# Optimization experiments

Hardware: AMD Instinct MI355X
Metric: run time of the kernel (lower is better)

The kernel has to match this reference:

```python
import jax, jax.numpy as jnp
import numpy as np
from jax import lax

B, IN_N, MID_N, OUT_N, K, L, WH = 16, 256, 256, 256, 3, 4096, 1024
EPS = 1e-5


def att_conv(x, W, b=None):
    # x: [B, Cin, L], W: [B, Cout, Cin, K] -> per-sample conv1d, padding='same'
    pl, pr = (K - 1) // 2, K // 2
    xp = jnp.pad(x, ((0, 0), (0, 0), (pl, pr)))
    out = 0.
    for t in range(K):  # small fixed K, unrolled shifted-slice einsum
        out = out + jnp.einsum('bcl,boc->bol', lax.dynamic_slice_in_dim(xp, t, L, 2), W[..., t])
    if b is not None:
        out = out + b[:, :, None]
    return out


def batch_norm(x, w, b):
    # training-mode BN over (N, L) per channel, biased variance
    mean = x.mean((0, 2), keepdims=True)
    var = ((x - mean) ** 2).mean((0, 2), keepdims=True)
    return (x - mean) * (w[None, :, None] / jnp.sqrt(var + EPS)) + b[None, :, None]


def se_module(x, w1, b1, w2, b2):
    s = x.mean(2, keepdims=True)  # [B, C, 1]
    s = jax.nn.relu(jnp.einsum('bcl,oc->bol', s, w1) + b1[None, :, None])
    s = jax.nn.sigmoid(jnp.einsum('bcl,oc->bol', s, w2) + b2[None, :, None])
    return x * s


def setup_inputs() -> dict:
    key = jax.random.key(0)
    ks = jax.random.split(key, 16)
    f = lambda k, sh, sc=0.02: jax.random.normal(k, sh, jnp.float32) * sc
    return {
        'x': f(ks[0], (B, IN_N, L), 1.0),
        'att1': f(ks[1], (B, MID_N, WH), 1.0),
        'att2': f(ks[2], (B, MID_N, WH), 1.0),
        'att3': f(ks[3], (B, OUT_N, WH), 1.0),
        'w1_w': f(ks[4], (IN_N * K, WH)), 'w1_b': jnp.zeros((IN_N * K,), jnp.float32),
        'w2_w': f(ks[5], (MID_N * K, WH)), 'w2_b': jnp.zeros((MID_N * K,), jnp.float32),
        'w3_w': f(ks[6], (MID_N * K, WH)), 'w3_b': jnp.zeros((MID_N * K,), jnp.float32),
        'b1_w': f(ks[7], (1, WH)), 'b1_b': jnp.zeros((1,), jnp.float32),
        'bn2_w': jnp.full((MID_N,), 0.1, jnp.float32), 'bn2_b': jnp.zeros((MID_N,), jnp.float32),
        'bn3_w': jnp.full((OUT_N,), 0.1, jnp.float32), 'bn3_b': jnp.zeros((OUT_N,), jnp.float32),
        'se1_w': f(ks[8], (OUT_N, OUT_N)), 'se1_b': jnp.zeros((OUT_N,), jnp.float32),
        'se2_w': f(ks[9], (OUT_N, OUT_N)), 'se2_b': jnp.zeros((OUT_N,), jnp.float32),
    }


def reference(x, att1, att2, att3, w1_w, w1_b, w2_w, w2_b, w3_w, w3_b,
              b1_w, b1_b, bn2_w, bn2_b, bn3_w, bn3_b, se1_w, se1_b, se2_w, se2_b):
    shortcut = x  # in_n == out_n, no downsample -> Identity
    # hypernetwork weight generation (Linear on last dim)
    W1 = (att1 @ w1_w.T + w1_b).reshape(B, MID_N, IN_N, K)
    W2 = (att2 @ w2_w.T + w2_b).reshape(B, MID_N, MID_N, K)
    W3 = (att3 @ w3_w.T + w3_b).reshape(B, OUT_N, MID_N, K)
    b1 = (att1 @ b1_w.T + b1_b)[..., 0]  # [B, mid_n]
    h = jax.nn.relu(att_conv(x, W1, b1))
    h = jax.nn.relu(batch_norm(att_conv(h, W2), bn2_w, bn2_b))
    h = jax.nn.relu(batch_norm(att_conv(h, W3), bn3_w, bn3_b))
    out = jax.nn.relu(se_module(h, se1_w, se1_b, se2_w, se2_b) + shortcut)
    return out
```

## Files before the change

### kernel.cpp

```cpp
#include <hip/hip_runtime.h>
#include <hip/hip_bf16.h>

using bf16 = __hip_bfloat16;
typedef __attribute__((ext_vector_type(4))) float f32x4;
typedef __attribute__((ext_vector_type(8))) short short8;
typedef __attribute__((ext_vector_type(2))) unsigned int uint2v;
typedef __attribute__((ext_vector_type(4))) unsigned int uint4v;

#define DEVI static __device__ __forceinline__

DEVI unsigned short f2b(float f){
  unsigned int u = __float_as_uint(f);
  unsigned int r = (u + 0x7fffu + ((u >> 16) & 1u)) >> 16;
  return (unsigned short)r;
}
DEVI float b2f(unsigned short u){
  return __uint_as_float(((unsigned int)u) << 16);
}

DEVI void gload16(const void* g, void* l){
  __builtin_amdgcn_global_load_lds(
      (const __attribute__((address_space(1))) unsigned int*)g,
      (__attribute__((address_space(3))) unsigned int*)l, 16, 0, 0);
}

__global__ __launch_bounds__(256) void k_transpose_x(const float* __restrict__ x,
                                                     bf16* __restrict__ xt)
{
  __shared__ float tile[64][65];
  const int b = blockIdx.z, l0 = blockIdx.x*64, c0 = blockIdx.y*64;
  const int tid = threadIdx.x;
  {
    const int r = tid >> 2, q = tid & 3;
    const float* src = x + ((size_t)(b*256 + c0 + r))*4096 + l0 + q*16;
    #pragma unroll
    for (int j = 0; j < 4; ++j){
      const f32x4 v = *reinterpret_cast<const f32x4*>(src + j*4);
      #pragma unroll
      for (int e = 0; e < 4; ++e) tile[r][q*16 + j*4 + e] = v[e];
    }
  }
  __syncthreads();
  {
    const int jr = tid >> 2, cq = tid & 3;
    unsigned int w[8];
    #pragma unroll
    for (int e = 0; e < 8; ++e){
      const float lo = tile[cq*16 + 2*e][jr];
      const float hi = tile[cq*16 + 2*e + 1][jr];
      w[e] = (unsigned int)f2b(lo) | ((unsigned int)f2b(hi) << 16);
    }
    unsigned short* dst = (unsigned short*)xt + ((size_t)b*4098 + l0 + jr + 1)*256 + c0 + cq*16;
    uint4v a0 = {w[0],w[1],w[2],w[3]}, a1 = {w[4],w[5],w[6],w[7]};
    *reinterpret_cast<uint4v*>(dst)     = a0;
    *reinterpret_cast<uint4v*>(dst + 8) = a1;
  }
}

__global__ void k_zero_pads(bf16* __restrict__ xt, bf16* __restrict__ h1t)
{
  const int b = blockIdx.x, tid = threadIdx.x;
  const size_t top = (size_t)b*4098*256 + tid;
  const size_t bot = (size_t)b*4098*256 + (size_t)4097*256 + tid;
  unsigned short* px = (unsigned short*)xt;
  unsigned short* ph = (unsigned short*)h1t;
  px[top] = 0; px[bot] = 0; ph[top] = 0; ph[bot] = 0;
}

__global__ __launch_bounds__(256) void k_cvt3(const float* __restrict__ s0, const float* __restrict__ s1,
                                              const float* __restrict__ s2, bf16* __restrict__ dst, int n1)
{
  const size_t total = (size_t)3 * (size_t)n1 / 4;
  for (size_t i = (size_t)blockIdx.x*256 + threadIdx.x; i < total; i += (size_t)gridDim.x*256){
    const size_t e = i*4;
    const int which = (int)(e / (size_t)n1);
    const size_t off = e - (size_t)which*(size_t)n1;
    const float* s = which==0 ? s0 : which==1 ? s1 : s2;
    const f32x4 v = *reinterpret_cast<const f32x4*>(s + off);
    uint2v p;
    p[0] = (unsigned)f2b(v[0]) | ((unsigned)f2b(v[1])<<16);
    p[1] = (unsigned)f2b(v[2]) | ((unsigned)f2b(v[3])<<16);
    *reinterpret_cast<uint2v*>((unsigned short*)dst + e) = p;
  }
}

__global__ __launch_bounds__(512, 2) void k_gen(const float* __restrict__ att1f, const float* __restrict__ att2f,
                                                const float* __restrict__ att3f, const bf16* __restrict__ wbp,
                                                const float* __restrict__ bias0, const float* __restrict__ bias1,
                                                const float* __restrict__ bias2, bf16* __restrict__ Wt)
{
  __shared__ bf16 sAll[32768];
  const int flat = blockIdx.x + (blockIdx.z << 4);
  const int xcd = flat & 7, s = flat >> 3;
  const int t = s % 3, tau = (s/3)*8 + xcd;
  const int i = tau >> 4, bo = tau & 15;
  const int bo0 = bo*256;
  const bf16*  __restrict__ A  = wbp + (size_t)i*768*1024 + (size_t)t*1024;
  const float* __restrict__ Bf = ((i==0) ? att1f : (i==1) ? att2f : att3f) + (size_t)bo0*1024;
  const float* __restrict__ bias = (i==0) ? bias0 : (i==1) ? bias1 : bias2;
  const int tid = threadIdx.x, lane = tid & 63, wid = tid >> 6;
  const int wr = wid >> 2, wc = wid & 3;
  const int frow = lane & 15, g = lane >> 4;
  f32x4 acc[8][4] = {};
  f32x4 rN[4];

  const int rB = tid >> 1, hB = tid & 1;
  const float* bsBase = Bf + (size_t)rB*1024 + hB*16;

#define GEN_STAGE_A(kt, bufi) { \
    _Pragma("unroll") \
    for (int j = 0; j < 2; ++j){ \
      const int q = tid + j*512, r = q >> 2, s3 = q & 3; \
      const int cc = (s3 ^ ((r >> 1) & 3)) * 8; \
      gload16(A + (size_t)r*3072 + (kt)*32 + cc, &sAll[(bufi)*8192 + q*8]); \
    } }

#define GEN_WRITE_B(bufi) { \
    unsigned short* wp = (unsigned short*)&sAll[16384 + (bufi)*8192]; \
    uint4v w0, w1; \
    w0[0] = (unsigned)f2b(rN[0][0]) | ((unsigned)f2b(rN[0][1])<<16); \
    w0[1] = (unsigned)f2b(rN[0][2]) | ((unsigned)f2b(rN[0][3])<<16); \
    w0[2] = (unsigned)f2b(rN[1][0]) | ((unsigned)f2b(rN[1][1])<<16); \
    w0[3] = (unsigned)f2b(rN[1][2]) | ((unsigned)f2b(rN[1][3])<<16); \
    w1[0] = (unsigned)f2b(rN[2][0]) | ((unsigned)f2b(rN[2][1])<<16); \
    w1[1] = (unsigned)f2b(rN[2][2]) | ((unsigned)f2b(rN[2][3])<<16); \
    w1[2] = (unsigned)f2b(rN[3][0]) | ((unsigned)f2b(rN[3][1])<<16); \
    w1[3] = (unsigned)f2b(rN[3][2]) | ((unsigned)f2b(rN[3][3])<<16); \
    const int sl0 = (hB*2 + 0) ^ ((rB >> 1) & 3); \
    const int sl1 = (hB*2 + 1) ^ ((rB >> 1) & 3); \
    *reinterpret_cast<uint4v*>(wp + rB*32 + sl0*8) = w0; \
    *reinterpret_cast<uint4v*>(wp + rB*32 + sl1*8) = w1; }

  #pragma unroll
  for (int q = 0; q < 4; ++q) rN[q] = *reinterpret_cast<const f32x4*>(bsBase + q*4);
  GEN_STAGE_A(0, 0);
  asm volatile("s_waitcnt vmcnt(0)" ::: "memory");
  GEN_WRITE_B(0);
  asm volatile("s_waitcnt lgkmcnt(0)" ::: "memory");
  __builtin_amdgcn_s_barrier();

  #pragma unroll 1
  for (int kt = 0; kt < 32; ++kt){
    const int p = kt & 1;
    if (kt + 1 < 32){
      #pragma unroll
      for (int q = 0; q < 4; ++q) rN[q] = *reinterpret_cast<const f32x4*>(bsBase + (kt+1)*32 + q*4);
      GEN_STAGE_A(kt+1, p^1);
      asm volatile("s_waitcnt vmcnt(10)" ::: "memory");
    } else {
      asm volatile("s_waitcnt vmcnt(0)" ::: "memory");
    }
    __builtin_amdgcn_s_barrier();
    const bf16* pA = sAll + p*8192;
    const bf16* pB = sAll + 16384 + p*8192;
    short8 bfr[4];
    #pragma unroll
    for (int n = 0; n < 4; ++n){
      const int row = wc*64 + n*16 + frow;
      const int sl = g ^ ((row >> 1) & 3);
      bfr[n] = *reinterpret_cast<const short8*>(pB + row*32 + sl*8);
    }
    __builtin_amdgcn_s_setprio(1);
    #pragma unroll
    for (int m = 0; m < 8; ++m){
      const int row = wr*128 + m*16 + frow;
      const int sl = g ^ ((row >> 1) & 3);
      const short8 af = *reinterpret_cast<const short8*>(pA + row*32 + sl*8);
      #pragma unroll
      for (int n = 0; n < 4; ++n)
        acc[m][n] = __builtin_amdgcn_mfma_f32_16x16x32_bf16(af, bfr[n], acc[m][n], 0, 0, 0);
    }
    __builtin_amdgcn_s_setprio(0);
    if (kt + 1 < 32){
      GEN_WRITE_B(p^1);
    }
    asm volatile("s_waitcnt lgkmcnt(0)" ::: "memory");
    __builtin_amdgcn_s_barrier();
  }
#undef GEN_STAGE_A
#undef GEN_WRITE_B

  char* gp = (char*)Wt + 2*(((size_t)(i*16 + bo)*3 + t)*65536);
  #pragma unroll
  for (int pass = 0; pass < 2; ++pass){
    if ((wc >> 1) == pass){
      #pragma unroll
      for (int m = 0; m < 8; ++m){
        const int col = wr*128 + m*16 + g*4;
        float bi[4];
        #pragma unroll
        for (int j = 0; j < 4; ++j) bi[j] = bias[(col + j)*3 + t];
        #pragma unroll
        for (int n = 0; n < 4; ++n){
          const int row = wc*64 + n*16 + frow;
          const int lrow = row & 127;
          uint2v pk;
          pk[0] = (unsigned)f2b(acc[m][n][0] + bi[0]) | ((unsigned)f2b(acc[m][n][1] + bi[1]) << 16);
          pk[1] = (unsigned)f2b(acc[m][n][2] + bi[2]) | ((unsigned)f2b(acc[m][n][3] + bi[3]) << 16);
          const int chunk = (col >> 3) ^ (lrow & 31);
          *reinterpret_cast<uint2v*>((char*)sAll + lrow*512 + chunk*16 + (g&1)*8) = pk;
        }
      }
    }
    __syncthreads();
    #pragma unroll
    for (int it = 0; it < 8; ++it){
      const int lrow = it*16 + (tid >> 5);
      const int c = tid & 31;
      const int cs2 = c ^ (lrow & 31);
      const uint4v v = *reinterpret_cast<const uint4v*>((const char*)sAll + lrow*512 + cs2*16);
      *reinterpret_cast<uint4v*>(gp + (size_t)(pass*128 + lrow)*512 + c*16) = v;
    }
    __syncthreads();
  }
}

__global__ __launch_bounds__(256) void k_b1(const float* __restrict__ att1, const float* __restrict__ b1w,
                                            const float* __restrict__ b1b, float* __restrict__ out)
{
  const int m = blockIdx.x*4 + (threadIdx.x >> 6);
  const int lane = threadIdx.x & 63;
  const float* a = att1 + (size_t)m*1024;
  float s = 0.f;
  for (int k = lane*4; k < 1024; k += 256){
    const f32x4 v = *reinterpret_cast<const f32x4*>(a + k);
    const f32x4 w = *reinterpret_cast<const f32x4*>(b1w + k);
    s += v[0]*w[0] + v[1]*w[1] + v[2]*w[2] + v[3]*w[3];
  }
  #pragma unroll
  for (int d = 32; d > 0; d >>= 1) s += __shfl_down(s, d);
  if (lane == 0) out[m] = s + b1b[0];
}

__global__ __launch_bounds__(512, 4) void k_conv(const bf16* __restrict__ Xt, const bf16* __restrict__ W,
                                                 const float* __restrict__ bias, bf16* __restrict__ out,
                                                 int outBatchStride, int outRowOff, int applyRelu,
                                                 float* __restrict__ statSum, float* __restrict__ statSq)
{
  __shared__ bf16 sAll[32768];
  const int flat = blockIdx.x + (blockIdx.z << 5);
  const int xcd = flat & 7, slot = flat >> 3;
  const int b = 2*xcd + (slot >> 5);
  const int l0 = (slot & 31) * 128;
  const int tid = threadIdx.x, lane = tid & 63, wid = tid >> 6;
  const int wr = wid >> 1, wc = wid & 1;
  const int frow = lane & 15, g = lane >> 4;
  f32x4 acc[4][4] = {};

#define CONV_STAGE(kt, bufi) { \
    const int ct3 = (kt)/3, tt = (kt) - ct3*3, c0 = ct3*32; \
    const bf16* Ab = W  + (((size_t)b*3 + tt)*256)*256 + c0; \
    const bf16* Bb = Xt + ((size_t)b*4098 + l0 + tt)*256 + c0; \
    _Pragma("unroll") \
    for (int j = 0; j < 2; ++j){ \
      const int q = tid + j*512, r = q >> 2, s3 = q & 3; \
      const int cc = (s3 ^ ((r >> 1) & 3)) * 8; \
      gload16(Ab + (size_t)r*256 + cc, &sAll[(bufi)*8192 + q*8]); \
    } \
    { const int q = tid, r = q >> 2, s3 = q & 3; \
      const int cc = (s3 ^ ((r >> 1) & 3)) * 8; \
      gload16(Bb + (size_t)r*256 + cc, &sAll[16384 + (bufi)*4096 + q*8]); } \
  }

  CONV_STAGE(0, 0);
  #pragma unroll 1
  for (int kt = 0; kt < 24; ++kt){
    const int buf = kt & 1;
    if (kt + 1 < 24){
      CONV_STAGE(kt+1, buf^1);
      asm volatile("s_waitcnt vmcnt(3)" ::: "memory");
    } else {
      asm volatile("s_waitcnt vmcnt(0)" ::: "memory");
    }
    __builtin_amdgcn_s_barrier();
    const bf16* pA = sAll + buf*8192;
    const bf16* pB = sAll + 16384 + buf*4096;
    short8 bfr[4], afr[4];
    #pragma unroll
    for (int n = 0; n < 4; ++n){
      const int row = wc*64 + n*16 + frow;
      const int sl = g ^ ((row >> 1) & 3);
      bfr[n] = *reinterpret_cast<const short8*>(pB + row*32 + sl*8);
    }
    #pragma unroll
    for (int m = 0; m < 4; ++m){
      const int row = wr*64 + m*16 + frow;
      const int sl = g ^ ((row >> 1) & 3);
      afr[m] = *reinterpret_cast<const short8*>(pA + row*32 + sl*8);
    }
    __builtin_amdgcn_s_setprio(1);
    #pragma unroll
    for (int m = 0; m < 4; ++m)
      #pragma unroll
      for (int n = 0; n < 4; ++n)
        acc[m][n] = __builtin_amdgcn_mfma_f32_16x16x32_bf16(afr[m], bfr[n], acc[m][n], 0, 0, 0);
    __builtin_amdgcn_s_setprio(0);
    __builtin_amdgcn_s_barrier();
  }
#undef CONV_STAGE

  float cs[4][4] = {{0.f}}, cq[4][4] = {{0.f}};
  #pragma unroll
  for (int m = 0; m < 4; ++m){
    const int col = wr*64 + m*16 + g*4;
    float bi[4] = {0.f, 0.f, 0.f, 0.f};
    if (bias){
      const f32x4 bv = *reinterpret_cast<const f32x4*>(bias + b*256 + col);
      bi[0]=bv[0]; bi[1]=bv[1]; bi[2]=bv[2]; bi[3]=bv[3];
    }
    #pragma unroll
    for (int n = 0; n < 4; ++n){
      const int row = wc*64 + n*16 + frow;
      float v[4];
      #pragma unroll
      for (int j = 0; j < 4; ++j){
        v[j] = acc[m][n][j] + bi[j];
        if (applyRelu) v[j] = fmaxf(v[j], 0.f);
        cs[m][j] += v[j];
        cq[m][j] += v[j]*v[j];
      }
      uint2v pk;
      pk[0] = (unsigned)f2b(v[0]) | ((unsigned)f2b(v[1]) << 16);
      pk[1] = (unsigned)f2b(v[2]) | ((unsigned)f2b(v[3]) << 16);
      const int chunk = (col >> 3) ^ (row & 31);
      *reinterpret_cast<uint2v*>((char*)sAll + row*512 + chunk*16 + (g&1)*8) = pk;
    }
  }
  __syncthreads();
  {
    char* gp = (char*)out + 2*((size_t)b*outBatchStride + (size_t)(l0 + outRowOff)*256);
    #pragma unroll
    for (int it = 0; it < 8; ++it){
      const int row = it*16 + (tid >> 5);
      const int c = tid & 31;
      const int cs2 = c ^ (row & 31);
      const uint4v v = *reinterpret_cast<const uint4v*>((const char*)sAll + row*512 + cs2*16);
      *reinterpret_cast<uint4v*>(gp + (size_t)row*512 + c*16) = v;
    }
  }
  if (statSum){
    #pragma unroll
    for (int m = 0; m < 4; ++m)
      #pragma unroll
      for (int j = 0; j < 4; ++j){
        #pragma unroll
        for (int d = 1; d < 16; d <<= 1){
          cs[m][j] += __shfl_xor(cs[m][j], d);
          cq[m][j] += __shfl_xor(cq[m][j], d);
        }
      }
    __syncthreads();
    float* ls = (float*)sAll;
    float* lq = ls + 512;
    if (frow == 0){
      #pragma unroll
      for (int m = 0; m < 4; ++m)
        #pragma unroll
        for (int j = 0; j < 4; ++j){
          ls[wid*64 + m*16 + g*4 + j] = cs[m][j];
          lq[wid*64 + m*16 + g*4 + j] = cq[m][j];
        }
    }
    __syncthreads();
    if (tid < 256){
      const int o = tid, wrI = o >> 6, idx = o & 63;
      const float s  = ls[(wrI*2 + 0)*64 + idx] + ls[(wrI*2 + 1)*64 + idx];
      const float qq = lq[(wrI*2 + 0)*64 + idx] + lq[(wrI*2 + 1)*64 + idx];
      atomicAdd(statSum + o, s);
      atomicAdd(statSq  + o, qq);
    }
  }
}

__global__ void k_bnfin(const float* __restrict__ sum, const float* __restrict__ sq,
                        const float* __restrict__ g, const float* __restrict__ bb,
                        float* __restrict__ scale, float* __restrict__ shift)
{
  const int o = threadIdx.x;
  const float inv = 1.f/65536.f;
  const float m = sum[o]*inv;
  const float v = fmaxf(sq[o]*inv - m*m, 0.f);
  const float sc = g[o] / sqrtf(v + 1e-5f);
  scale[o] = sc;
  shift[o] = bb[o] - m*sc;
}

__global__ __launch_bounds__(256) void k_norm2(const bf16* __restrict__ y, const float* __restrict__ scale,
                                               const float* __restrict__ shift, bf16* __restrict__ h)
{
  const int gr = blockIdx.x*8 + (threadIdx.x >> 5);
  const int oc = threadIdx.x & 31;
  const int b = gr / 4098, lp = gr - b*4098;
  unsigned short* dst = (unsigned short*)h + (size_t)gr*256 + oc*8;
  if (lp == 0 || lp == 4097){
    uint4v z = {0u,0u,0u,0u};
    *reinterpret_cast<uint4v*>(dst) = z;
    return;
  }
  const unsigned short* src = (const unsigned short*)y + ((size_t)b*4096 + (lp-1))*256 + oc*8;
  const uint4v in = *reinterpret_cast<const uint4v*>(src);
  const f32x4 sA0 = *reinterpret_cast<const f32x4*>(scale + oc*8);
  const f32x4 sA1 = *reinterpret_cast<const f32x4*>(scale + oc*8 + 4);
  const f32x4 hA0 = *reinterpret_cast<const f32x4*>(shift + oc*8);
  const f32x4 hA1 = *reinterpret_cast<const f32x4*>(shift + oc*8 + 4);
  uint4v ov;
  #pragma unroll
  for (int e = 0; e < 4; ++e){
    const unsigned int w = in[e];
    const float sc0 = (e<2) ? sA0[2*e] : sA1[2*e-4];
    const float sc1 = (e<2) ? sA0[2*e+1] : sA1[2*e-3];
    const float sh0 = (e<2) ? hA0[2*e] : hA1[2*e-4];
    const float sh1 = (e<2) ? hA0[2*e+1] : hA1[2*e-3];
    const float v0 = fmaxf(b2f((unsigned short)(w & 0xffffu))*sc0 + sh0, 0.f);
    const float v1 = fmaxf(b2f((unsigned short)(w >> 16))*sc1 + sh1, 0.f);
    ov[e] = (unsigned)f2b(v0) | ((unsigned)f2b(v1) << 16);
  }
  *reinterpret_cast<uint4v*>(dst) = ov;
}

__global__ __launch_bounds__(256) void k_norm3(bf16* __restrict__ y, const float* __restrict__ scale,
                                               const float* __restrict__ shift, float* __restrict__ s_sum)
{
  __shared__ float red[8][256];
  const int tid = threadIdx.x;
  const int rr = tid >> 5, oc = tid & 31;
  const size_t row = (size_t)blockIdx.x*8 + rr;
  const int b = (int)(row >> 12);
  unsigned short* p = (unsigned short*)y + row*256 + oc*8;
  const uint4v in = *reinterpret_cast<const uint4v*>(p);
  const f32x4 sA0 = *reinterpret_cast<const f32x4*>(scale + oc*8);
  const f32x4 sA1 = *reinterpret_cast<const f32x4*>(scale + oc*8 + 4);
  const f32x4 hA0 = *reinterpret_cast<const f32x4*>(shift + oc*8);
  const f32x4 hA1 = *reinterpret_cast<const f32x4*>(shift + oc*8 + 4);
  uint4v ov;
  float loc[8];
  #pragma unroll
  for (int e = 0; e < 4; ++e){
    const unsigned int w = in[e];
    const float sc0 = (e<2) ? sA0[2*e] : sA1[2*e-4];
    const float sc1 = (e<2) ? sA0[2*e+1] : sA1[2*e-3];
    const float sh0 = (e<2) ? hA0[2*e] : hA1[2*e-4];
    const float sh1 = (e<2) ? hA0[2*e+1] : hA1[2*e-3];
    const float v0 = fmaxf(b2f((unsigned short)(w & 0xffffu))*sc0 + sh0, 0.f);
    const float v1 = fmaxf(b2f((unsigned short)(w >> 16))*sc1 + sh1, 0.f);
    loc[2*e] = v0; loc[2*e+1] = v1;
    ov[e] = (unsigned)f2b(v0) | ((unsigned)f2b(v1) << 16);
  }
  *reinterpret_cast<uint4v*>(p) = ov;
  #pragma unroll
  for (int j = 0; j < 8; ++j) red[rr][oc*8 + j] = loc[j];
  __syncthreads();
  const int o = tid;
  float tot = 0.f;
  #pragma unroll
  for (int r2 = 0; r2 < 8; ++r2) tot += red[r2][o];
  atomicAdd(&s_sum[(size_t)b*256 + o], tot);
}

__global__ __launch_bounds__(256) void k_se(const float* __restrict__ s_sum, const float* __restrict__ w1,
                                            const float* __restrict__ b1, const float* __restrict__ w2,
                                            const float* __restrict__ b2, float* __restrict__ s2)
{
  __shared__ float sv[256];
  __shared__ float t1[256];
  const int b = blockIdx.x, o = threadIdx.x;
  sv[o] = s_sum[(size_t)b*256 + o] * (1.f/4096.f);
  __syncthreads();
  float a = b1[o];
  for (int c = 0; c < 256; ++c) a += w1[(size_t)o*256 + c] * sv[c];
  t1[o] = fmaxf(a, 0.f);
  __syncthreads();
  float a2 = b2[o];
  for (int c = 0; c < 256; ++c) a2 += w2[(size_t)o*256 + c] * t1[c];
  s2[(size_t)b*256 + o] = 1.f / (1.f + expf(-a2));
}

__global__ __launch_bounds__(256) void k_final(const bf16* __restrict__ h3, const float* __restrict__ s2,
                                               const float* __restrict__ x, float* __restrict__ out)
{
  __shared__ float tile[64][65];
  const int b = blockIdx.z, o0 = blockIdx.y*64, l0 = blockIdx.x*64;
  const int tid = threadIdx.x;
  {
    const int r = tid >> 2, q = tid & 3;
    const unsigned short* src = (const unsigned short*)h3 + ((size_t)b*4096 + l0 + r)*256 + o0 + q*16;
    const uint4v a0 = *reinterpret_cast<const uint4v*>(src);
    const uint4v a1 = *reinterpret_cast<const uint4v*>(src + 8);
    #pragma unroll
    for (int e = 0; e < 4; ++e){
      tile[r][q*16 + 2*e]         = b2f((unsigned short)(a0[e] & 0xffffu));
      tile[r][q*16 + 2*e + 1]     = b2f((unsigned short)(a0[e] >> 16));
      tile[r][q*16 + 8 + 2*e]     = b2f((unsigned short)(a1[e] & 0xffffu));
      tile[r][q*16 + 8 + 2*e + 1] = b2f((unsigned short)(a1[e] >> 16));
    }
  }
  __syncthreads();
  {
    const int orow = tid >> 2, q = tid & 3;
    const int o = o0 + orow;
    const float sc = s2[(size_t)b*256 + o];
    const float* xs = x + ((size_t)b*256 + o)*4096 + l0 + q*16;
    float* dst = out + ((size_t)b*256 + o)*4096 + l0 + q*16;
    #pragma unroll
    for (int k = 0; k < 16; k += 4){
      const f32x4 xv = *reinterpret_cast<const f32x4*>(xs + k);
      f32x4 r;
      #pragma unroll
      for (int e = 0; e < 4; ++e)
        r[e] = fmaxf(tile[q*16 + k + e][orow]*sc + xv[e], 0.f);
      *reinterpret_cast<f32x4*>(dst + k) = r;
    }
  }
}

extern "C" void kernel_launch(void* const* d_in, const int* in_sizes, int n_in,
                              void* d_out, int out_size, void* d_ws, size_t ws_size,
                              hipStream_t stream)
{
  const float* x     = (const float*)d_in[0];
  const float* att1  = (const float*)d_in[1];
  const float* att2  = (const float*)d_in[2];
  const float* att3  = (const float*)d_in[3];
  const float* w1_w  = (const float*)d_in[4];
  const float* w1_b  = (const float*)d_in[5];
  const float* w2_w  = (const float*)d_in[6];
  const float* w2_b  = (const float*)d_in[7];
  const float* w3_w  = (const float*)d_in[8];
  const float* w3_b  = (const float*)d_in[9];
  const float* b1_w  = (const float*)d_in[10];
  const float* b1_b  = (const float*)d_in[11];
  const float* bn2_w = (const float*)d_in[12];
  const float* bn2_b = (const float*)d_in[13];
  const float* bn3_w = (const float*)d_in[14];
  const float* bn3_b = (const float*)d_in[15];
  const float* se1_w = (const float*)d_in[16];
  const float* se1_b = (const float*)d_in[17];
  const float* se2_w = (const float*)d_in[18];
  const float* se2_b = (const float*)d_in[19];

  char* ws = (char*)d_ws;
  bf16*  xT   = (bf16*)(ws + 0);
  bf16*  h1T  = (bf16*)(ws + 33570816);
  bf16*  y2T  = (bf16*)(ws + 67141632);
  bf16*  h2T  = (bf16*)(ws + 100696064);
  bf16*  Wt   = (bf16*)(ws + 134266880);
  bf16*  wb   = (bf16*)(ws + 178307072);
  float* b1v  = (float*)(ws + 183025664);
  float* st   = (float*)(ws + 183042048);
  float* bn2sum = st;
  float* bn2sq  = st + 256;
  float* bn3sum = st + 512;
  float* bn3sq  = st + 768;
  float* s_sum  = st + 1024;
  float* scale2 = st + 5120;
  float* shift2 = st + 5376;
  float* scale3 = st + 5632;
  float* shift3 = st + 5888;
  float* s2v    = st + 6144;
  bf16*  y3T  = (bf16*)(ws + 0);

  hipMemsetAsync(st, 0, 5120*sizeof(float), stream);

  k_transpose_x<<<dim3(64,4,16),256,0,stream>>>(x, xT);
  k_zero_pads<<<16,256,0,stream>>>(xT, h1T);
  k_cvt3<<<512,256,0,stream>>>(w1_w, w2_w, w3_w, wb, 768*1024);
  k_gen<<<dim3(16,1,9),512,0,stream>>>(att1, att2, att3, wb, w1_b, w2_b, w3_b, Wt);
  k_b1<<<1024,256,0,stream>>>(att1, b1_w, b1_b, b1v);

  k_conv<<<dim3(32,1,16),512,0,stream>>>(xT,  Wt,                           b1v,     h1T, 4098*256, 1, 1, nullptr, nullptr);
  k_conv<<<dim3(32,1,16),512,0,stream>>>(h1T, Wt + (size_t)1*16*3*256*256,  nullptr, y2T, 4096*256, 0, 0, bn2sum, bn2sq);
  k_bnfin<<<1,256,0,stream>>>(bn2sum, bn2sq, bn2_w, bn2_b, scale2, shift2);
  k_norm2<<<8196,256,0,stream>>>(y2T, scale2, shift2, h2T);
  k_conv<<<dim3(32,1,16),512,0,stream>>>(h2T, Wt + (size_t)2*16*3*256*256,  nullptr, y3T, 4096*256, 0, 0, bn3sum, bn3sq);
  k_bnfin<<<1,256,0,stream>>>(bn3sum, bn3sq, bn3_w, bn3_b, scale3, shift3);
  k_norm3<<<8192,256,0,stream>>>(y3T, scale3, shift3, s_sum);
  k_se<<<16,256,0,stream>>>(s_sum, se1_w, se1_b, se2_w, se2_b, s2v);
  k_final<<<dim3(64,4,16),256,0,stream>>>((const bf16*)y3T, s2v, x, (float*)d_out);
}
```

Baseline: 326.9 us.

## Halve k_gen tile, load fp32 att via direct-to-LDS, convert at fragment read

The hypernetwork weight-generation GEMM now uses 256x128 output tiles instead of 256x256, doubling the grid to 288 blocks and raising the occupancy hint to 4 blocks per CU. The fp32 attention operand is loaded straight into LDS with async global-to-LDS loads and converted to bf16 with v_cvt_pk_bf16_f32 when fragments are read, replacing the register-staged convert-and-write path. The epilogue becomes a single pass. This aims to fill more CUs and cut register pressure and LDS write overhead. In exchange each block reuses the weight tile over less output, and it adds per-kt conversion work and larger fp32 LDS traffic for B.

```diff
diff --git a/kernel.cpp b/kernel.cpp
--- a/kernel.cpp
+++ b/kernel.cpp
@@ -84,134 +84,112 @@
   }
 }
 
-__global__ __launch_bounds__(512, 2) void k_gen(const float* __restrict__ att1f, const float* __restrict__ att2f,
+__global__ __launch_bounds__(512, 4) void k_gen(const float* __restrict__ att1f, const float* __restrict__ att2f,
                                                 const float* __restrict__ att3f, const bf16* __restrict__ wbp,
                                                 const float* __restrict__ bias0, const float* __restrict__ bias1,
                                                 const float* __restrict__ bias2, bf16* __restrict__ Wt)
 {
   __shared__ bf16 sAll[32768];
-  const int flat = blockIdx.x + (blockIdx.z << 4);
+  const int flat = blockIdx.x + (blockIdx.z << 5);
   const int xcd = flat & 7, s = flat >> 3;
-  const int t = s % 3, tau = (s/3)*8 + xcd;
-  const int i = tau >> 4, bo = tau & 15;
-  const int bo0 = bo*256;
+  const int t = s % 3, u = s / 3;
+  const int tau = u*8 + xcd;
+  const int i = tau >> 5, boc = tau & 31;
+  const int bo0 = boc*128;
   const bf16*  __restrict__ A  = wbp + (size_t)i*768*1024 + (size_t)t*1024;
   const float* __restrict__ Bf = ((i==0) ? att1f : (i==1) ? att2f : att3f) + (size_t)bo0*1024;
   const float* __restrict__ bias = (i==0) ? bias0 : (i==1) ? bias1 : bias2;
   const int tid = threadIdx.x, lane = tid & 63, wid = tid >> 6;
-  const int wr = wid >> 2, wc = wid & 3;
+  const int wr = wid >> 1, wc = wid & 1;
   const int frow = lane & 15, g = lane >> 4;
-  f32x4 acc[8][4] = {};
-  f32x4 rN[4];
-
-  const int rB = tid >> 1, hB = tid & 1;
-  const float* bsBase = Bf + (size_t)rB*1024 + hB*16;
-
-#define GEN_STAGE_A(kt, bufi) { \
+  f32x4 acc[4][4] = {};
+
+#define GEN_STAGE(kt, bufi) { \
     _Pragma("unroll") \
     for (int j = 0; j < 2; ++j){ \
       const int q = tid + j*512, r = q >> 2, s3 = q & 3; \
       const int cc = (s3 ^ ((r >> 1) & 3)) * 8; \
-      gload16(A + (size_t)r*3072 + (kt)*32 + cc, &sAll[(bufi)*8192 + q*8]); \
-    } }
-
-#define GEN_WRITE_B(bufi) { \
-    unsigned short* wp = (unsigned short*)&sAll[16384 + (bufi)*8192]; \
-    uint4v w0, w1; \
-    w0[0] = (unsigned)f2b(rN[0][0]) | ((unsigned)f2b(rN[0][1])<<16); \
-    w0[1] = (unsigned)f2b(rN[0][2]) | ((unsigned)f2b(rN[0][3])<<16); \
-    w0[2] = (unsigned)f2b(rN[1][0]) | ((unsigned)f2b(rN[1][1])<<16); \
-    w0[3] = (unsigned)f2b(rN[1][2]) | ((unsigned)f2b(rN[1][3])<<16); \
-    w1[0] = (unsigned)f2b(rN[2][0]) | ((unsigned)f2b(rN[2][1])<<16); \
-    w1[1] = (unsigned)f2b(rN[2][2]) | ((unsigned)f2b(rN[2][3])<<16); \
-    w1[2] = (unsigned)f2b(rN[3][0]) | ((unsigned)f2b(rN[3][1])<<16); \
-    w1[3] = (unsigned)f2b(rN[3][2]) | ((unsigned)f2b(rN[3][3])<<16); \
-    const int sl0 = (hB*2 + 0) ^ ((rB >> 1) & 3); \
-    const int sl1 = (hB*2 + 1) ^ ((rB >> 1) & 3); \
-    *reinterpret_cast<uint4v*>(wp + rB*32 + sl0*8) = w0; \
-    *reinterpret_cast<uint4v*>(wp + rB*32 + sl1*8) = w1; }
-
-  #pragma unroll
-  for (int q = 0; q < 4; ++q) rN[q] = *reinterpret_cast<const f32x4*>(bsBase + q*4);
-  GEN_STAGE_A(0, 0);
-  asm volatile("s_waitcnt vmcnt(0)" ::: "memory");
-  GEN_WRITE_B(0);
-  asm volatile("s_waitcnt lgkmcnt(0)" ::: "memory");
-  __builtin_amdgcn_s_barrier();
-
+      gload16(A + (size_t)r*3072 + (kt)*32 + cc, (char*)sAll + (bufi)*16384 + q*16); \
+    } \
+    _Pragma("unroll") \
+    for (int j = 0; j < 2; ++j){ \
+      const int q = tid + j*512, r = q >> 3, s7 = q & 7; \
+      const int ss = s7 ^ (r & 7); \
+      gload16(Bf + (size_t)r*1024 + (kt)*32 + ss*4, (char*)sAll + 32768 + (bufi)*16384 + q*16); \
+    } \
+  }
+
+  GEN_STAGE(0, 0);
   #pragma unroll 1
   for (int kt = 0; kt < 32; ++kt){
     const int p = kt & 1;
     if (kt + 1 < 32){
-      #pragma unroll
-      for (int q = 0; q < 4; ++q) rN[q] = *reinterpret_cast<const f32x4*>(bsBase + (kt+1)*32 + q*4);
-      GEN_STAGE_A(kt+1, p^1);
-      asm volatile("s_waitcnt vmcnt(10)" ::: "memory");
+      GEN_STAGE(kt+1, p^1);
+      asm volatile("s_waitcnt vmcnt(4)" ::: "memory");
     } else {
       asm volatile("s_waitcnt vmcnt(0)" ::: "memory");
     }
     __builtin_amdgcn_s_barrier();
-    const bf16* pA = sAll + p*8192;
-    const bf16* pB = sAll + 16384 + p*8192;
+    const char* pA = (const char*)sAll + p*16384;
+    const char* pB = (const char*)sAll + 32768 + p*16384;
     short8 bfr[4];
     #pragma unroll
     for (int n = 0; n < 4; ++n){
       const int row = wc*64 + n*16 + frow;
+      const f32x4 f0 = *reinterpret_cast<const f32x4*>(pB + row*128 + (((2*g)  ^ (row & 7))*16));
+      const f32x4 f1 = *reinterpret_cast<const f32x4*>(pB + row*128 + (((2*g+1)^ (row & 7))*16));
+      unsigned int w0, w1, w2, w3;
+      asm("v_cvt_pk_bf16_f32 %0, %1, %2" : "=v"(w0) : "v"(f0[0]), "v"(f0[1]));
+      asm("v_cvt_pk_bf16_f32 %0, %1, %2" : "=v"(w1) : "v"(f0[2]), "v"(f0[3]));
+      asm("v_cvt_pk_bf16_f32 %0, %1, %2" : "=v"(w2) : "v"(f1[0]), "v"(f1[1]));
+      asm("v_cvt_pk_bf16_f32 %0, %1, %2" : "=v"(w3) : "v"(f1[2]), "v"(f1[3]));
+      union { uint4v u; short8 sv; } cvtu;
+      cvtu.u[0] = w0; cvtu.u[1] = w1; cvtu.u[2] = w2; cvtu.u[3] = w3;
+      bfr[n] = cvtu.sv;
+    }
+    __builtin_amdgcn_s_setprio(1);
+    #pragma unroll
+    for (int m = 0; m < 4; ++m){
+      const int row = wr*64 + m*16 + frow;
       const int sl = g ^ ((row >> 1) & 3);
-      bfr[n] = *reinterpret_cast<const short8*>(pB + row*32 + sl*8);
-    }
-    __builtin_amdgcn_s_setprio(1);
-    #pragma unroll
-    for (int m = 0; m < 8; ++m){
-      const int row = wr*128 + m*16 + frow;
-      const int sl = g ^ ((row >> 1) & 3);
-      const short8 af = *reinterpret_cast<const short8*>(pA + row*32 + sl*8);
+      const short8 af = *reinterpret_cast<const short8*>(pA + row*64 + sl*16);
       #pragma unroll
       for (int n = 0; n < 4; ++n)
         acc[m][n] = __builtin_amdgcn_mfma_f32_16x16x32_bf16(af, bfr[n], acc[m][n], 0, 0, 0);
     }
     __builtin_amdgcn_s_setprio(0);
-    if (kt + 1 < 32){
-      GEN_WRITE_B(p^1);
-    }
-    asm volatile("s_waitcnt lgkmcnt(0)" ::: "memory");
     __builtin_amdgcn_s_barrier();
   }
-#undef GEN_STAGE_A
-#undef GEN_WRITE_B
-
-  char* gp = (char*)Wt + 2*(((size_t)(i*16 + bo)*3 + t)*65536);
-  #pragma unroll
-  for (int pass = 0; pass < 2; ++pass){
-    if ((wc >> 1) == pass){
-      #pragma unroll
-      for (int m = 0; m < 8; ++m){
-        const int col = wr*128 + m*16 + g*4;
-        float bi[4];
-        #pragma unroll
-        for (int j = 0; j < 4; ++j) bi[j] = bias[(col + j)*3 + t];
-        #pragma unroll
-        for (int n = 0; n < 4; ++n){
-          const int row = wc*64 + n*16 + frow;
-          const int lrow = row & 127;
-          uint2v pk;
-          pk[0] = (unsigned)f2b(acc[m][n][0] + bi[0]) | ((unsigned)f2b(acc[m][n][1] + bi[1]) << 16);
-          pk[1] = (unsigned)f2b(acc[m][n][2] + bi[2]) | ((unsigned)f2b(acc[m][n][3] + bi[3]) << 16);
-          const int chunk = (col >> 3) ^ (lrow & 31);
-          *reinterpret_cast<uint2v*>((char*)sAll + lrow*512 + chunk*16 + (g&1)*8) = pk;
-        }
-      }
-    }
-    __syncthreads();
+#undef GEN_STAGE
+
+  #pragma unroll
+  for (int m = 0; m < 4; ++m){
+    const int col = wr*64 + m*16 + g*4;
+    float bi[4];
+    #pragma unroll
+    for (int j = 0; j < 4; ++j) bi[j] = bias[(col + j)*3 + t];
+    #pragma unroll
+    for (int n = 0; n < 4; ++n){
+      const int row = wc*64 + n*16 + frow;
+      uint2v pk;
+      pk[0] = (unsigned)f2b(acc[m][n][0] + bi[0]) | ((unsigned)f2b(acc[m][n][1] + bi[1]) << 16);
+      pk[1] = (unsigned)f2b(acc[m][n][2] + bi[2]) | ((unsigned)f2b(acc[m][n][3] + bi[3]) << 16);
+      const int chunk = (col >> 3) ^ (row & 31);
+      *reinterpret_cast<uint2v*>((char*)sAll + row*512 + chunk*16 + (g&1)*8) = pk;
+    }
+  }
+  __syncthreads();
+  {
+    const int bb = boc >> 1, o0 = (boc & 1)*128;
+    char* gp = (char*)Wt + 2*((((size_t)(i*16 + bb)*3 + t)*256 + o0)*256);
     #pragma unroll
     for (int it = 0; it < 8; ++it){
-      const int lrow = it*16 + (tid >> 5);
+      const int row = it*16 + (tid >> 5);
       const int c = tid & 31;
-      const int cs2 = c ^ (lrow & 31);
-      const uint4v v = *reinterpret_cast<const uint4v*>((const char*)sAll + lrow*512 + cs2*16);
-      *reinterpret_cast<uint4v*>(gp + (size_t)(pass*128 + lrow)*512 + c*16) = v;
-    }
-    __syncthreads();
+      const int cs2 = c ^ (row & 31);
+      const uint4v v = *reinterpret_cast<const uint4v*>((const char*)sAll + row*512 + cs2*16);
+      *reinterpret_cast<uint4v*>(gp + (size_t)row*512 + c*16) = v;
+    }
   }
 }
 
@@ -564,7 +542,7 @@
   k_transpose_x<<<dim3(64,4,16),256,0,stream>>>(x, xT);
   k_zero_pads<<<16,256,0,stream>>>(xT, h1T);
   k_cvt3<<<512,256,0,stream>>>(w1_w, w2_w, w3_w, wb, 768*1024);
-  k_gen<<<dim3(16,1,9),512,0,stream>>>(att1, att2, att3, wb, w1_b, w2_b, w3_b, Wt);
+  k_gen<<<dim3(32,1,9),512,0,stream>>>(att1, att2, att3, wb, w1_b, w2_b, w3_b, Wt);
   k_b1<<<1024,256,0,stream>>>(att1, b1_w, b1_b, b1v);
 
   k_conv<<<dim3(32,1,16),512,0,stream>>>(xT,  Wt,                           b1v,     h1T, 4098*256, 1, 1, nullptr, nullptr);
```

New measurement: 310.8 us. 1.05x faster.
